# Optimization experiments

Measured on AMD Instinct MI355X. Metric: run time of the kernel, lower is better.

## Reference

```python
import jax, jax.numpy as jnp
import numpy as np

B, T, N_EMBED = 16, 4096, 48
HEAD_SIZE, DIM = 8, 64  # dim = 2**n_wires, n_wires = 6


def setup_inputs() -> dict:
    key = jax.random.key(0)
    k1, k2, k3 = jax.random.split(key, 3)
    x = jax.random.normal(k1, (B, T, N_EMBED), dtype=jnp.float32)
    obs_re = jax.random.normal(k2, (HEAD_SIZE, DIM, DIM), dtype=jnp.float32)
    obs_im = jax.random.normal(k3, (HEAD_SIZE, DIM, DIM), dtype=jnp.float32)
    return {"x": x, "obs_re": obs_re, "obs_im": obs_im}


def reference(x, obs_re, obs_im):
    # x: (B, T, C) real; obs: (H, dim, dim) complex observables O'.
    b, t, c = x.shape
    h, dim, _ = obs_re.shape
    O = (obs_re + 1j * obs_im).astype(jnp.complex64)  # (h, dim, dim)
    # psi: zero-padded complex state, x loaded into first n_embed amplitudes
    psi = jnp.zeros((b * t, dim), dtype=jnp.complex64)
    psi = psi.at[:, :c].set(x.reshape(b * t, c).astype(jnp.complex64))
    # O_psi[h, n, i] = sum_j O[h, i, j] * psi[n, j]  (all heads in one batched GEMM)
    O_psi = jnp.einsum('hij,nj->hni', O, psi)
    # exp[n, h] = Re( psi^H O' psi )
    exp = jnp.einsum('ni,hni->nh', jnp.conj(psi), O_psi).real
    return exp.reshape(b, t, h).astype(jnp.float32)
```

## Files before the change

### kernel.cpp

```cpp
#include <hip/hip_runtime.h>


#define NTOK 65536
#define CDIM 48
#define ODIM 64
#define NHEAD 8
#define XSTRIDE 56

typedef __attribute__((ext_vector_type(8))) short short8;
typedef __attribute__((ext_vector_type(4))) short short4v;
typedef __attribute__((ext_vector_type(4))) float float4v;

static __device__ __forceinline__ short f2bf(float f) {
    unsigned int u = __builtin_bit_cast(unsigned int, f);
    u += 0x7FFFu + ((u >> 16) & 1u);
    return (short)(u >> 16);
}
static __device__ __forceinline__ float bf2f(short s) {
    return __builtin_bit_cast(float, ((unsigned int)(unsigned short)s) << 16);
}

__global__ __launch_bounds__(256) void prep_obs(const float* __restrict__ obs,
                                                short* __restrict__ ws) {
    int g = blockIdx.x * 256 + threadIdx.x;
    int f = g >> 6, lane = g & 63;
    int h = f / 6, rem = f % 6, kt = rem / 3, it = rem % 3;
    int q = lane >> 4, c = lane & 15;
    int i = 16 * it + c;
    int j0 = 32 * kt + 8 * q;
    const float* src = obs + ((size_t)(h * ODIM + i) * ODIM + j0);
    short8 v;
    #pragma unroll
    for (int jj = 0; jj < 8; ++jj) v[jj] = f2bf(src[jj]);
    *(short8*)(ws + ((size_t)f * 64 + lane) * 8) = v;
}

static __device__ __forceinline__ void head_compute(
    const short8 A[6], const short8 bfr[2], const float xe[3][4],
    float* __restrict__ out, int obase, int h, int lane)
{
    float4v acc[3];
    #pragma unroll
    for (int it = 0; it < 3; ++it) {
        float4v z = {0.f, 0.f, 0.f, 0.f};
        acc[it] = __builtin_amdgcn_mfma_f32_16x16x32_bf16(A[it],     bfr[0], z,       0, 0, 0);
        acc[it] = __builtin_amdgcn_mfma_f32_16x16x32_bf16(A[3 + it], bfr[1], acc[it], 0, 0, 0);
    }
    float p = 0.f;
    #pragma unroll
    for (int it = 0; it < 3; ++it)
        #pragma unroll
        for (int r = 0; r < 4; ++r)
            p += acc[it][r] * xe[it][r];
    p += __shfl_xor(p, 16, 64);
    p += __shfl_xor(p, 32, 64);
    if (lane < 16) out[obase + h] = p;
}

__global__ __launch_bounds__(256) void qform_mfma(const float* __restrict__ x,
                                                  const short* __restrict__ ws,
                                                  float* __restrict__ out) {
    __shared__ short xl[64 * XSTRIDE];
    const int tid = threadIdx.x;
    const int tb = blockIdx.x * 64;

    #pragma unroll
    for (int s = 0; s < 3; ++s) {
        int idx = s * 256 + tid;
        int t = idx / 12, ch = idx % 12;
        float4 v = ((const float4*)x)[(size_t)tb * 12 + idx];
        short4v b;
        b.x = f2bf(v.x); b.y = f2bf(v.y); b.z = f2bf(v.z); b.w = f2bf(v.w);
        *(short4v*)(xl + t * XSTRIDE + ch * 4) = b;
    }
    __syncthreads();

    const int w = tid >> 6, lane = tid & 63;
    const int q = lane >> 4, c = lane & 15;
    const int row = w * 16 + c;

    short8 bfr[2];
    bfr[0] = *(const short8*)(xl + row * XSTRIDE + q * 8);
    if (q < 2)
        bfr[1] = *(const short8*)(xl + row * XSTRIDE + q * 8 + 32);
    else
        bfr[1] = (short8)0;

    float xe[3][4];
    #pragma unroll
    for (int it = 0; it < 3; ++it)
        #pragma unroll
        for (int r = 0; r < 4; ++r)
            xe[it][r] = bf2f(xl[row * XSTRIDE + 16 * it + 4 * q + r]);

    const short8* aw = (const short8*)ws;
    const int obase = (tb + w * 16 + c) * NHEAD;

    short8 A0[6], A1[6];
    #pragma unroll
    for (int u = 0; u < 6; ++u) A0[u] = aw[u * 64 + lane];

    for (int h = 0; h < 8; h += 2) {
        #pragma unroll
        for (int u = 0; u < 6; ++u) A1[u] = aw[((h + 1) * 6 + u) * 64 + lane];
        head_compute(A0, bfr, xe, out, obase, h, lane);
        #pragma unroll
        for (int u = 0; u < 6; ++u) A0[u] = aw[(((h + 2) & 7) * 6 + u) * 64 + lane];
        head_compute(A1, bfr, xe, out, obase, h + 1, lane);
    }
}

extern "C" void kernel_launch(void* const* d_in, const int* in_sizes, int n_in,
                              void* d_out, int out_size, void* d_ws, size_t ws_size,
                              hipStream_t stream) {
    const float* x      = (const float*)d_in[0];
    const float* obs_re = (const float*)d_in[1];
    float* out = (float*)d_out;
    short* ws  = (short*)d_ws;

    prep_obs<<<12, 256, 0, stream>>>(obs_re, ws);
    qform_mfma<<<NTOK / 64, 256, 0, stream>>>(x, ws, out);
}
```

Before: 71.98 us.

## Fuse observable bf16 conversion into main kernel and stage fragments in LDS

Removes the separate prep_obs launch. Each block now converts the observable matrices to bf16 MFMA fragments itself and stores them in shared memory, so heads are read from LDS rather than from global workspace. Each block handles 128 tokens (two 16-token groups per wave) so every A fragment is reused twice, and the eight head results are written with two float4 stores. In exchange, every block repeats the obs conversion (48 fragments) and uses about 62KB of LDS, which limits occupancy.

```diff
diff --git a/kernel.cpp b/kernel.cpp
--- a/kernel.cpp
+++ b/kernel.cpp
@@ -2,10 +2,9 @@
 
 
 #define NTOK 65536
-#define CDIM 48
-#define ODIM 64
 #define NHEAD 8
 #define XSTRIDE 56
+#define TPB 128
 
 typedef __attribute__((ext_vector_type(8))) short short8;
 typedef __attribute__((ext_vector_type(4))) short short4v;
@@ -20,52 +19,34 @@
     return __builtin_bit_cast(float, ((unsigned int)(unsigned short)s) << 16);
 }
 
-__global__ __launch_bounds__(256) void prep_obs(const float* __restrict__ obs,
-                                                short* __restrict__ ws) {
-    int g = blockIdx.x * 256 + threadIdx.x;
-    int f = g >> 6, lane = g & 63;
-    int h = f / 6, rem = f % 6, kt = rem / 3, it = rem % 3;
-    int q = lane >> 4, c = lane & 15;
-    int i = 16 * it + c;
-    int j0 = 32 * kt + 8 * q;
-    const float* src = obs + ((size_t)(h * ODIM + i) * ODIM + j0);
-    short8 v;
-    #pragma unroll
-    for (int jj = 0; jj < 8; ++jj) v[jj] = f2bf(src[jj]);
-    *(short8*)(ws + ((size_t)f * 64 + lane) * 8) = v;
-}
+__global__ __launch_bounds__(256, 2) void qform_fused(
+    const float* __restrict__ x,
+    const float* __restrict__ obs,
+    float* __restrict__ out)
+{
+    __shared__ short a_lds[48 * 64 * 8];
+    __shared__ short xl[TPB * XSTRIDE];
 
-static __device__ __forceinline__ void head_compute(
-    const short8 A[6], const short8 bfr[2], const float xe[3][4],
-    float* __restrict__ out, int obase, int h, int lane)
-{
-    float4v acc[3];
-    #pragma unroll
-    for (int it = 0; it < 3; ++it) {
-        float4v z = {0.f, 0.f, 0.f, 0.f};
-        acc[it] = __builtin_amdgcn_mfma_f32_16x16x32_bf16(A[it],     bfr[0], z,       0, 0, 0);
-        acc[it] = __builtin_amdgcn_mfma_f32_16x16x32_bf16(A[3 + it], bfr[1], acc[it], 0, 0, 0);
-    }
-    float p = 0.f;
-    #pragma unroll
-    for (int it = 0; it < 3; ++it)
-        #pragma unroll
-        for (int r = 0; r < 4; ++r)
-            p += acc[it][r] * xe[it][r];
-    p += __shfl_xor(p, 16, 64);
-    p += __shfl_xor(p, 32, 64);
-    if (lane < 16) out[obase + h] = p;
-}
-
-__global__ __launch_bounds__(256) void qform_mfma(const float* __restrict__ x,
-                                                  const short* __restrict__ ws,
-                                                  float* __restrict__ out) {
-    __shared__ short xl[64 * XSTRIDE];
-    const int tid = threadIdx.x;
-    const int tb = blockIdx.x * 64;
+    const int tid  = threadIdx.x;
+    const int w    = tid >> 6, lane = tid & 63;
+    const int q    = lane >> 4, c = lane & 15;
+    const int tb   = blockIdx.x * TPB;
 
     #pragma unroll
-    for (int s = 0; s < 3; ++s) {
+    for (int u = 0; u < 12; ++u) {
+        int f = u * 4 + w;
+        int h = f / 6, rem = f % 6, kt = rem / 3, it = rem % 3;
+        const float4* src = (const float4*)(obs +
+            ((size_t)(h * 64 + 16 * it + c) * 64 + 32 * kt + 8 * q));
+        float4 v0 = src[0], v1 = src[1];
+        short8 a;
+        a[0] = f2bf(v0.x); a[1] = f2bf(v0.y); a[2] = f2bf(v0.z); a[3] = f2bf(v0.w);
+        a[4] = f2bf(v1.x); a[5] = f2bf(v1.y); a[6] = f2bf(v1.z); a[7] = f2bf(v1.w);
+        *(short8*)(a_lds + ((size_t)f * 64 + lane) * 8) = a;
+    }
+
+    #pragma unroll
+    for (int s = 0; s < 6; ++s) {
         int idx = s * 256 + tid;
         int t = idx / 12, ch = idx % 12;
         float4 v = ((const float4*)x)[(size_t)tb * 12 + idx];
@@ -75,38 +56,58 @@
     }
     __syncthreads();
 
-    const int w = tid >> 6, lane = tid & 63;
-    const int q = lane >> 4, c = lane & 15;
-    const int row = w * 16 + c;
+    short8 bfr[2][2];
+    float  xe[2][3][4];
+    #pragma unroll
+    for (int g = 0; g < 2; ++g) {
+        const int row = w * 32 + g * 16 + c;
+        bfr[g][0] = *(const short8*)(xl + row * XSTRIDE + q * 8);
+        if (q < 2)
+            bfr[g][1] = *(const short8*)(xl + row * XSTRIDE + 32 + q * 8);
+        else
+            bfr[g][1] = (short8)0;
+        #pragma unroll
+        for (int it = 0; it < 3; ++it)
+            #pragma unroll
+            for (int r = 0; r < 4; ++r)
+                xe[g][it][r] = bf2f(xl[row * XSTRIDE + 16 * it + 4 * q + r]);
+    }
 
-    short8 bfr[2];
-    bfr[0] = *(const short8*)(xl + row * XSTRIDE + q * 8);
-    if (q < 2)
-        bfr[1] = *(const short8*)(xl + row * XSTRIDE + q * 8 + 32);
-    else
-        bfr[1] = (short8)0;
+    float ph[2][NHEAD];
+    #pragma unroll
+    for (int h = 0; h < NHEAD; ++h) {
+        short8 A[6];
+        #pragma unroll
+        for (int u = 0; u < 6; ++u)
+            A[u] = *(const short8*)(a_lds + ((size_t)(h * 6 + u) * 64 + lane) * 8);
+        #pragma unroll
+        for (int g = 0; g < 2; ++g) {
+            float4v acc[3];
+            #pragma unroll
+            for (int it = 0; it < 3; ++it) {
+                float4v z = {0.f, 0.f, 0.f, 0.f};
+                acc[it] = __builtin_amdgcn_mfma_f32_16x16x32_bf16(A[it],     bfr[g][0], z,       0, 0, 0);
+                acc[it] = __builtin_amdgcn_mfma_f32_16x16x32_bf16(A[3 + it], bfr[g][1], acc[it], 0, 0, 0);
+            }
+            float p = 0.f;
+            #pragma unroll
+            for (int it = 0; it < 3; ++it)
+                #pragma unroll
+                for (int r = 0; r < 4; ++r)
+                    p += acc[it][r] * xe[g][it][r];
+            p += __shfl_xor(p, 16, 64);
+            p += __shfl_xor(p, 32, 64);
+            ph[g][h] = p;
+        }
+    }
 
-    float xe[3][4];
-    #pragma unroll
-    for (int it = 0; it < 3; ++it)
+    if (lane < 16) {
         #pragma unroll
-        for (int r = 0; r < 4; ++r)
-            xe[it][r] = bf2f(xl[row * XSTRIDE + 16 * it + 4 * q + r]);
-
-    const short8* aw = (const short8*)ws;
-    const int obase = (tb + w * 16 + c) * NHEAD;
-
-    short8 A0[6], A1[6];
-    #pragma unroll
-    for (int u = 0; u < 6; ++u) A0[u] = aw[u * 64 + lane];
-
-    for (int h = 0; h < 8; h += 2) {
-        #pragma unroll
-        for (int u = 0; u < 6; ++u) A1[u] = aw[((h + 1) * 6 + u) * 64 + lane];
-        head_compute(A0, bfr, xe, out, obase, h, lane);
-        #pragma unroll
-        for (int u = 0; u < 6; ++u) A0[u] = aw[(((h + 2) & 7) * 6 + u) * 64 + lane];
-        head_compute(A1, bfr, xe, out, obase, h + 1, lane);
+        for (int g = 0; g < 2; ++g) {
+            float4* o4 = (float4*)(out + (size_t)(tb + w * 32 + g * 16 + c) * NHEAD);
+            o4[0] = make_float4(ph[g][0], ph[g][1], ph[g][2], ph[g][3]);
+            o4[1] = make_float4(ph[g][4], ph[g][5], ph[g][6], ph[g][7]);
+        }
     }
 }
 
@@ -116,8 +117,6 @@
     const float* x      = (const float*)d_in[0];
     const float* obs_re = (const float*)d_in[1];
     float* out = (float*)d_out;
-    short* ws  = (short*)d_ws;
 
-    prep_obs<<<12, 256, 0, stream>>>(obs_re, ws);
-    qform_mfma<<<NTOK / 64, 256, 0, stream>>>(x, ws, out);
+    qform_fused<<<NTOK / TPB, 256, 0, stream>>>(x, obs_re, out);
 }
```

After: 71.87 us. About the same (-0.2%).
